# Performance work log

Hardware: AMD Instinct MI355X
Metric: run time of the kernel (lower is better)

Reference implementation:

```python
import math
import jax, jax.numpy as jnp
import numpy as np

N_HEAD = 12
LN_EPS = 1e-5

def _gelu(x):
    # NewGELU: tanh approximation
    c = math.sqrt(2.0 / math.pi)
    return 0.5 * x * (1.0 + jnp.tanh(c * (x + 0.044715 * x ** 3)))

def _ln(x, w, b):
    m = x.mean(-1, keepdims=True)
    v = x.var(-1, keepdims=True)
    return (x - m) / jnp.sqrt(v + LN_EPS) * w + b

def setup_inputs() -> dict:
    key = jax.random.key(0)
    ks = jax.random.split(key, 8)
    L, C, V, BS = 12, 768, 30522, 1024
    B, T = 4, 1024
    std = 0.02
    inp = {
        'idx': jax.random.randint(ks[0], (B, T), 0, V),
        'wte': jax.random.normal(ks[1], (V, C), jnp.float32) * std,
        'wpe': jax.random.normal(ks[2], (BS, C), jnp.float32) * std,
        'ln1_w': jnp.ones((L, C), jnp.float32),
        'ln1_b': jnp.zeros((L, C), jnp.float32),
        'attn_w': jax.random.normal(ks[3], (L, 3 * C, C), jnp.float32) * std,
        'attn_b': jnp.zeros((L, 3 * C), jnp.float32),
        'proj_w': jax.random.normal(ks[4], (L, C, C), jnp.float32) * (std / math.sqrt(2 * L)),
        'proj_b': jnp.zeros((L, C), jnp.float32),
        'ln2_w': jnp.ones((L, C), jnp.float32),
        'ln2_b': jnp.zeros((L, C), jnp.float32),
        'fc_w': jax.random.normal(ks[5], (L, 4 * C, C), jnp.float32) * std,
        'fc_b': jnp.zeros((L, 4 * C), jnp.float32),
        'mproj_w': jax.random.normal(ks[6], (L, C, 4 * C), jnp.float32) * (std / math.sqrt(2 * L)),
        'mproj_b': jnp.zeros((L, C), jnp.float32),
        'lnf_w': jnp.ones((C,), jnp.float32),
        'lnf_b': jnp.zeros((C,), jnp.float32),
        'lm_head_w': jax.random.normal(ks[7], (V, C), jnp.float32) * std,
    }
    return inp

def reference(idx, wte, wpe, ln1_w, ln1_b, attn_w, attn_b, proj_w, proj_b,
              ln2_w, ln2_b, fc_w, fc_b, mproj_w, mproj_b, lnf_w, lnf_b, lm_head_w):
    B, T = idx.shape
    C = wte.shape[1]
    H = N_HEAD
    D = C // H
    scale = 1.0 / math.sqrt(D)
    x = wte[idx] + wpe[:T][None]  # [B,T,C], drop is identity (p=0)

    def block(x, p):
        l1w, l1b, aw, ab, pw, pb, l2w, l2b, fw, fb, mw, mb = p
        h = _ln(x, l1w, l1b)
        qkv = jnp.einsum('btc,ec->bte', h, aw) + ab  # [B,T,3C]
        q, k, v = jnp.split(qkv, 3, axis=-1)
        q = q.reshape(B, T, H, D)
        k = k.reshape(B, T, H, D)
        v = v.reshape(B, T, H, D)
        att = jnp.einsum('bthd,bshd->bhts', q, k) * scale  # [B,H,T,T]
        att = jax.nn.softmax(att, axis=-1)  # mask=None: full attention
        y = jnp.einsum('bhts,bshd->bthd', att, v).reshape(B, T, C)
        x = x + jnp.einsum('btc,oc->bto', y, pw) + pb
        h = _gelu(jnp.einsum('btc,fc->btf', _ln(x, l2w, l2b), fw) + fb)
        x = x + jnp.einsum('btf,cf->btc', h, mw) + mb
        return x, None

    x, _ = jax.lax.scan(block, x, (ln1_w, ln1_b, attn_w, attn_b, proj_w, proj_b,
                                   ln2_w, ln2_b, fc_w, fc_b, mproj_w, mproj_b))
    x = _ln(x, lnf_w, lnf_b)
    logits = jnp.einsum('btc,vc->btv', x, lm_head_w)  # [B,T,V]
    return logits
```

## Files before the change

### kernel.cpp

```cpp
#include <hip/hip_runtime.h>
#include <hip/hip_bf16.h>
#include <math.h>

typedef __attribute__((ext_vector_type(8))) short short8;
typedef __attribute__((ext_vector_type(4))) float f32x4;

typedef unsigned short u16;

__device__ __forceinline__ u16 f2bf(float f) {
    union { float f; unsigned int u; } v; v.f = f;
    unsigned int u = v.u;
    unsigned int r = (u + 0x7fffu + ((u >> 16) & 1u)) >> 16;
    return (u16)r;
}
__device__ __forceinline__ float bf2f(u16 u) {
    union { unsigned int u; float f; } v; v.u = ((unsigned int)u) << 16;
    return v.f;
}

__device__ __forceinline__ void gload16(const void* g, void* l) {
    __builtin_amdgcn_global_load_lds(
        (const __attribute__((address_space(1))) void*)g,
        (__attribute__((address_space(3))) void*)l, 16, 0, 0);
}

__global__ __launch_bounds__(256) void castw_kernel(const float* __restrict__ src,
                                                    u16* __restrict__ dst,
                                                    long n, long npad) {
    long i = ((long)blockIdx.x * 256 + threadIdx.x) * 4;
    const long stride = (long)gridDim.x * 1024;
    for (; i < npad; i += stride) {
        ushort4 o;
        if (i < n) {
            float4 v = *reinterpret_cast<const float4*>(src + i);
            o.x = f2bf(v.x); o.y = f2bf(v.y); o.z = f2bf(v.z); o.w = f2bf(v.w);
        } else {
            o = make_ushort4(0, 0, 0, 0);
        }
        *reinterpret_cast<ushort4*>(dst + i) = o;
    }
}

__global__ __launch_bounds__(256) void embed_kernel(const int* __restrict__ idx,
                                                    const float* __restrict__ wte,
                                                    const float* __restrict__ wpe,
                                                    float* __restrict__ x) {
    const int row = blockIdx.x;
    const int tid = threadIdx.x;
    const int t = row & 1023;
    const int tok = idx[row];
    const float* we = wte + (size_t)tok * 768;
    const float* pe = wpe + (size_t)t * 768;
    float* xr = x + (size_t)row * 768;
    xr[tid]       = we[tid]       + pe[tid];
    xr[tid + 256] = we[tid + 256] + pe[tid + 256];
    xr[tid + 512] = we[tid + 512] + pe[tid + 512];
}

__global__ __launch_bounds__(256) void ln_kernel(const float* __restrict__ x,
                                                 const float* __restrict__ w,
                                                 const float* __restrict__ b,
                                                 u16* __restrict__ out) {
    const int row = blockIdx.x;
    const int tid = threadIdx.x;
    const float* xr = x + (size_t)row * 768;
    float v0 = xr[tid], v1 = xr[tid + 256], v2 = xr[tid + 512];
    float s = v0 + v1 + v2;
    float q = v0 * v0 + v1 * v1 + v2 * v2;
    #pragma unroll
    for (int off = 32; off >= 1; off >>= 1) {
        s += __shfl_xor(s, off);
        q += __shfl_xor(q, off);
    }
    __shared__ float rs[4], rq[4];
    const int wid = tid >> 6, lane = tid & 63;
    if (lane == 0) { rs[wid] = s; rq[wid] = q; }
    __syncthreads();
    s = rs[0] + rs[1] + rs[2] + rs[3];
    q = rq[0] + rq[1] + rq[2] + rq[3];
    const float mean = s * (1.f / 768.f);
    const float var = q * (1.f / 768.f) - mean * mean;
    const float rstd = rsqrtf(var + 1e-5f);
    u16* orow = out + (size_t)row * 768;
    orow[tid]       = f2bf((v0 - mean) * rstd * w[tid]       + b[tid]);
    orow[tid + 256] = f2bf((v1 - mean) * rstd * w[tid + 256] + b[tid + 256]);
    orow[tid + 512] = f2bf((v2 - mean) * rstd * w[tid + 512] + b[tid + 512]);
}

template<int EPI>
__global__ __launch_bounds__(256) void gemm_bb(
        const u16* __restrict__ A, int lda,
        const u16* __restrict__ B, int ldb,
        const float* __restrict__ bias,
        void* __restrict__ Cout, int ldc,
        int N, int K, int nmt,
        float* __restrict__ resid) {
    __shared__ __align__(16) u16 lds[2][2][128 * 32];
    const int tid = threadIdx.x;
    const int lane = tid & 63, wid = tid >> 6;
    const int nwg = gridDim.x;
    const int o = blockIdx.x;
    const int wg = (o & 7) * (nwg >> 3) + (o >> 3);
    const int m0 = (wg % nmt) * 128, n0 = (wg / nmt) * 128;

    const int wm = (wid >> 1) * 64, wn = (wid & 1) * 64;
    const int l16 = lane & 15, lk = (lane >> 4) * 8;

    const size_t a_off0 = (size_t)(m0 + (tid >> 2)) * lda + (tid & 3) * 8;
    const size_t a_off1 = a_off0 + (size_t)64 * lda;
    const size_t b_off0 = (size_t)(n0 + (tid >> 2)) * ldb + (tid & 3) * 8;
    const size_t b_off1 = b_off0 + (size_t)64 * ldb;
    const int ldst = tid * 8;

    f32x4 acc[4][4];
    #pragma unroll
    for (int i = 0; i < 4; i++)
        #pragma unroll
        for (int j = 0; j < 4; j++)
            acc[i][j] = (f32x4){0.f, 0.f, 0.f, 0.f};

    const int nk = K >> 5;
    gload16(A + a_off0, lds[0][0] + ldst);
    gload16(A + a_off1, lds[0][0] + ldst + 2048);
    gload16(B + b_off0, lds[0][1] + ldst);
    gload16(B + b_off1, lds[0][1] + ldst + 2048);

    for (int t = 0; t < nk; ++t) {
        if (t + 1 < nk) {
            u16* Ap = lds[(t + 1) & 1][0];
            u16* Bp = lds[(t + 1) & 1][1];
            const int k0 = (t + 1) << 5;
            gload16(A + a_off0 + k0, Ap + ldst);
            gload16(A + a_off1 + k0, Ap + ldst + 2048);
            gload16(B + b_off0 + k0, Bp + ldst);
            gload16(B + b_off1 + k0, Bp + ldst + 2048);
            asm volatile("s_waitcnt vmcnt(4)" ::: "memory");
        } else {
            asm volatile("s_waitcnt vmcnt(0)" ::: "memory");
        }
        __builtin_amdgcn_s_barrier();
        asm volatile("" ::: "memory");
        const u16* As = lds[t & 1][0];
        const u16* Bs = lds[t & 1][1];
        short8 af[4], bf[4];
        #pragma unroll
        for (int i = 0; i < 4; i++) {
            af[i] = *reinterpret_cast<const short8*>(&As[(wm + i * 16 + l16) * 32 + lk]);
            bf[i] = *reinterpret_cast<const short8*>(&Bs[(wn + i * 16 + l16) * 32 + lk]);
        }
        #pragma unroll
        for (int mi = 0; mi < 4; mi++)
            #pragma unroll
            for (int ni = 0; ni < 4; ni++)
                acc[mi][ni] = __builtin_amdgcn_mfma_f32_16x16x32_bf16(af[mi], bf[ni], acc[mi][ni], 0, 0, 0);
        asm volatile("" ::: "memory");
        __builtin_amdgcn_s_barrier();
    }

    if (EPI == 3) {
        float* ct = reinterpret_cast<float*>(&lds[0][0][0]) + wid * 1088;
        const int rw = (lane >> 4) * 4;
        const int rr = lane >> 2;
        const int rc = (lane & 3) * 16;
        #pragma unroll
        for (int mi = 0; mi < 4; mi++) {
            asm volatile("" ::: "memory");
            #pragma unroll
            for (int ni = 0; ni < 4; ni++)
                #pragma unroll
                for (int j = 0; j < 4; j++)
                    ct[(rw + j) * 68 + ni * 16 + l16] = acc[mi][ni][j];
            asm volatile("" ::: "memory");
            const int m = m0 + wm + mi * 16 + rr;
            const int nb = n0 + wn + rc;
            float* crow = (float*)Cout + (size_t)m * ldc + nb;
            #pragma unroll
            for (int q = 0; q < 4; q++) {
                const f32x4 v = *reinterpret_cast<const f32x4*>(&ct[rr * 68 + rc + q * 4]);
                if (nb + q * 4 + 3 < N) {
                    *reinterpret_cast<f32x4*>(crow + q * 4) = v;
                } else {
                    #pragma unroll
                    for (int e = 0; e < 4; e++)
                        if (nb + q * 4 + e < N) crow[q * 4 + e] = v[e];
                }
            }
        }
    } else {
        const int cb = n0 + wn + l16;
        const int rb = m0 + wm + (lane >> 4) * 4;
        #pragma unroll
        for (int ni = 0; ni < 4; ni++) {
            const int n = cb + ni * 16;
            const float bv = bias[n];
            #pragma unroll
            for (int mi = 0; mi < 4; mi++) {
                #pragma unroll
                for (int j = 0; j < 4; j++) {
                    const int m = rb + mi * 16 + j;
                    float v = acc[mi][ni][j] + bv;
                    if (EPI == 0) {
                        ((u16*)Cout)[(size_t)m * ldc + n] = f2bf(v);
                    } else if (EPI == 1) {
                        resid[(size_t)m * ldc + n] += v;
                    } else {
                        const float t = tanhf(0.7978845608028654f * (v + 0.044715f * v * v * v));
                        ((u16*)Cout)[(size_t)m * ldc + n] = f2bf(0.5f * v * (1.f + t));
                    }
                }
            }
        }
    }
}

template<int EPI>
__global__ __launch_bounds__(256, 2) void gemm_bt(
        const u16* __restrict__ A, int lda,
        const float* __restrict__ B, int ldb,
        const float* __restrict__ bias,
        void* __restrict__ Cout, int ldc,
        int M, int N, int K,
        float* __restrict__ resid) {
    __shared__ __align__(16) u16 As[128][40];
    __shared__ __align__(16) u16 Bs[128][40];
    const int tid = threadIdx.x;
    const int lane = tid & 63, wid = tid >> 6;
    const int m0 = blockIdx.y * 128, n0 = blockIdx.x * 128;
    const int wm = (wid >> 1) * 64, wn = (wid & 1) * 64;
    const int l16 = lane & 15, lk = (lane >> 4) * 8;

    f32x4 acc[4][4];
    #pragma unroll
    for (int i = 0; i < 4; i++)
        #pragma unroll
        for (int j = 0; j < 4; j++)
            acc[i][j] = (f32x4){0.f, 0.f, 0.f, 0.f};

    for (int k0 = 0; k0 < K; k0 += 32) {
        #pragma unroll
        for (int p = 0; p < 2; p++) {
            const int e = p * 256 + tid;
            const int r = e >> 2, c = e & 3;
            uint4 v = *reinterpret_cast<const uint4*>(A + (size_t)(m0 + r) * lda + k0 + c * 8);
            *reinterpret_cast<uint4*>(&As[r][c * 8]) = v;
        }
        #pragma unroll
        for (int p = 0; p < 4; p++) {
            const int e = p * 256 + tid;
            const int r = e >> 3, c = e & 7;
            float4 v = make_float4(0.f, 0.f, 0.f, 0.f);
            if (n0 + r < N)
                v = *reinterpret_cast<const float4*>(B + (size_t)(n0 + r) * ldb + k0 + c * 4);
            ushort4 hv;
            hv.x = f2bf(v.x); hv.y = f2bf(v.y); hv.z = f2bf(v.z); hv.w = f2bf(v.w);
            *reinterpret_cast<ushort4*>(&Bs[r][c * 4]) = hv;
        }
        __syncthreads();
        short8 af[4], bfr[4];
        #pragma unroll
        for (int i = 0; i < 4; i++) {
            af[i]  = *reinterpret_cast<const short8*>(&As[wm + i * 16 + l16][lk]);
            bfr[i] = *reinterpret_cast<const short8*>(&Bs[wn + i * 16 + l16][lk]);
        }
        #pragma unroll
        for (int mi = 0; mi < 4; mi++)
            #pragma unroll
            for (int ni = 0; ni < 4; ni++)
                acc[mi][ni] = __builtin_amdgcn_mfma_f32_16x16x32_bf16(af[mi], bfr[ni], acc[mi][ni], 0, 0, 0);
        __syncthreads();
    }

    const int cb = n0 + wn + l16;
    const int rb = m0 + wm + (lane >> 4) * 4;
    #pragma unroll
    for (int ni = 0; ni < 4; ni++) {
        const int n = cb + ni * 16;
        if (n >= N) continue;
        float bv = 0.f;
        if (EPI != 3) bv = bias[n];
        #pragma unroll
        for (int mi = 0; mi < 4; mi++) {
            #pragma unroll
            for (int j = 0; j < 4; j++) {
                const int m = rb + mi * 16 + j;
                float v = acc[mi][ni][j] + bv;
                if (EPI == 0) {
                    ((u16*)Cout)[(size_t)m * ldc + n] = f2bf(v);
                } else if (EPI == 1) {
                    resid[(size_t)m * ldc + n] += v;
                } else if (EPI == 2) {
                    const float t = tanhf(0.7978845608028654f * (v + 0.044715f * v * v * v));
                    ((u16*)Cout)[(size_t)m * ldc + n] = f2bf(0.5f * v * (1.f + t));
                } else {
                    ((float*)Cout)[(size_t)m * ldc + n] = v;
                }
            }
        }
    }
}

__global__ __launch_bounds__(256, 2) void attn_mfma_kernel(const u16* __restrict__ qkv,
                                                           u16* __restrict__ y) {
    __shared__ __align__(16) u16 Qs[64][72];
    __shared__ __align__(16) u16 Ks[64][72];
    __shared__ __align__(16) u16 Vt[64][72];
    __shared__ __align__(16) u16 Ps[4][16][72];

    const int tid = threadIdx.x;
    const int lane = tid & 63, wid = tid >> 6;
    const int l16 = lane & 15, lk = (lane >> 4) * 8;
    const int qt = blockIdx.x, h = blockIdx.y, b = blockIdx.z;

    const size_t base = (size_t)b * 1024 * 2304;
    const u16* qp = qkv + base + (size_t)(qt * 64) * 2304 + h * 64;
    const u16* kp = qkv + base + 768  + h * 64;
    const u16* vp = qkv + base + 1536 + h * 64;

    #pragma unroll
    for (int p = 0; p < 2; p++) {
        const int e = p * 256 + tid;
        const int rr = e >> 3, c8 = e & 7;
        *reinterpret_cast<uint4*>(&Qs[rr][c8 * 8]) =
            *reinterpret_cast<const uint4*>(qp + (size_t)rr * 2304 + c8 * 8);
    }
    __syncthreads();

    short8 qf[2];
    #pragma unroll
    for (int kk = 0; kk < 2; kk++)
        qf[kk] = *reinterpret_cast<const short8*>(&Qs[wid * 16 + l16][kk * 32 + lk]);

    f32x4 o_acc[4];
    #pragma unroll
    for (int i = 0; i < 4; i++) o_acc[i] = (f32x4){0.f, 0.f, 0.f, 0.f};
    float l_part[4] = {0.f, 0.f, 0.f, 0.f};

    for (int s0 = 0; s0 < 1024; s0 += 64) {
        __syncthreads();
        #pragma unroll
        for (int p = 0; p < 2; p++) {
            const int e = p * 256 + tid;
            const int rr = e >> 3, c8 = e & 7;
            *reinterpret_cast<uint4*>(&Ks[rr][c8 * 8]) =
                *reinterpret_cast<const uint4*>(kp + (size_t)(s0 + rr) * 2304 + c8 * 8);
        }
        #pragma unroll
        for (int p = 0; p < 2; p++) {
            const int e = p * 256 + tid;
            const int s2 = e >> 4;
            const int dq = e & 15;
            const int s = s2 * 2;
            ushort4 v0 = *reinterpret_cast<const ushort4*>(vp + (size_t)(s0 + s) * 2304 + dq * 4);
            ushort4 v1 = *reinterpret_cast<const ushort4*>(vp + (size_t)(s0 + s + 1) * 2304 + dq * 4);
            *reinterpret_cast<ushort2*>(&Vt[dq * 4 + 0][s]) = make_ushort2(v0.x, v1.x);
            *reinterpret_cast<ushort2*>(&Vt[dq * 4 + 1][s]) = make_ushort2(v0.y, v1.y);
            *reinterpret_cast<ushort2*>(&Vt[dq * 4 + 2][s]) = make_ushort2(v0.z, v1.z);
            *reinterpret_cast<ushort2*>(&Vt[dq * 4 + 3][s]) = make_ushort2(v0.w, v1.w);
        }
        __syncthreads();

        f32x4 sa[4];
        #pragma unroll
        for (int i = 0; i < 4; i++) sa[i] = (f32x4){0.f, 0.f, 0.f, 0.f};
        #pragma unroll
        for (int nj = 0; nj < 4; nj++) {
            #pragma unroll
            for (int kk = 0; kk < 2; kk++) {
                short8 kf = *reinterpret_cast<const short8*>(&Ks[nj * 16 + l16][kk * 32 + lk]);
                sa[nj] = __builtin_amdgcn_mfma_f32_16x16x32_bf16(qf[kk], kf, sa[nj], 0, 0, 0);
            }
        }

        #pragma unroll
        for (int nj = 0; nj < 4; nj++) {
            #pragma unroll
            for (int r = 0; r < 4; r++) {
                const float pv = __expf(sa[nj][r] * 0.125f);
                l_part[r] += pv;
                Ps[wid][(lane >> 4) * 4 + r][nj * 16 + l16] = f2bf(pv);
            }
        }

        short8 pa[2];
        #pragma unroll
        for (int kk = 0; kk < 2; kk++)
            pa[kk] = *reinterpret_cast<const short8*>(&Ps[wid][l16][kk * 32 + lk]);
        #pragma unroll
        for (int nd = 0; nd < 4; nd++) {
            #pragma unroll
            for (int kk = 0; kk < 2; kk++) {
                short8 vf = *reinterpret_cast<const short8*>(&Vt[nd * 16 + l16][kk * 32 + lk]);
                o_acc[nd] = __builtin_amdgcn_mfma_f32_16x16x32_bf16(pa[kk], vf, o_acc[nd], 0, 0, 0);
            }
        }
    }

    float inv[4];
    #pragma unroll
    for (int r = 0; r < 4; r++) {
        float s = l_part[r];
        #pragma unroll
        for (int off = 8; off >= 1; off >>= 1) s += __shfl_xor(s, off);
        inv[r] = 1.f / s;
    }
    const int rowb = b * 1024 + qt * 64 + wid * 16 + (lane >> 4) * 4;
    #pragma unroll
    for (int nd = 0; nd < 4; nd++) {
        const int col = h * 64 + nd * 16 + l16;
        #pragma unroll
        for (int r = 0; r < 4; r++) {
            y[(size_t)(rowb + r) * 768 + col] = f2bf(o_acc[nd][r] * inv[r]);
        }
    }
}

extern "C" void kernel_launch(void* const* d_in, const int* in_sizes, int n_in,
                              void* d_out, int out_size, void* d_ws, size_t ws_size,
                              hipStream_t stream) {
    (void)in_sizes; (void)n_in; (void)out_size;
    const int*   idx    = (const int*)d_in[0];
    const float* wte    = (const float*)d_in[1];
    const float* wpe    = (const float*)d_in[2];
    const float* ln1w   = (const float*)d_in[3];
    const float* ln1b   = (const float*)d_in[4];
    const float* attnw  = (const float*)d_in[5];
    const float* attnb  = (const float*)d_in[6];
    const float* projw  = (const float*)d_in[7];
    const float* projb  = (const float*)d_in[8];
    const float* ln2w   = (const float*)d_in[9];
    const float* ln2b   = (const float*)d_in[10];
    const float* fcw    = (const float*)d_in[11];
    const float* fcb    = (const float*)d_in[12];
    const float* mprojw = (const float*)d_in[13];
    const float* mprojb = (const float*)d_in[14];
    const float* lnfw   = (const float*)d_in[15];
    const float* lnfb   = (const float*)d_in[16];
    const float* lmw    = (const float*)d_in[17];
    float* out = (float*)d_out;

    char* p = (char*)d_ws;
    size_t used = 0;
    auto take = [&](size_t bytes) { char* q = p + used; used += (bytes + 255) & ~(size_t)255; return q; };
    float* x      = (float*)take((size_t)4096 * 768 * 4);
    u16*   a_bf   = (u16*)take((size_t)4096 * 768 * 2);
    u16*   qkv_bf = (u16*)take((size_t)4096 * 2304 * 2);
    u16*   hid_bf = (u16*)take((size_t)4096 * 3072 * 2);
    u16*   w_lm   = (u16*)take((size_t)30592 * 768 * 2);
    const bool castLm = used <= ws_size;
    u16*   w_attn = (u16*)take((size_t)12 * 2304 * 768 * 2);
    u16*   w_proj = (u16*)take((size_t)12 * 768 * 768 * 2);
    u16*   w_fc   = (u16*)take((size_t)12 * 3072 * 768 * 2);
    u16*   w_mprj = (u16*)take((size_t)12 * 768 * 3072 * 2);
    const bool castAll = used <= ws_size;

    embed_kernel<<<4096, 256, 0, stream>>>(idx, wte, wpe, x);

    if (castLm)
        castw_kernel<<<2048, 256, 0, stream>>>(lmw, w_lm, (long)30522 * 768, (long)30592 * 768);
    if (castAll) {
        castw_kernel<<<2048, 256, 0, stream>>>(attnw,  w_attn, (long)12 * 2304 * 768, (long)12 * 2304 * 768);
        castw_kernel<<<2048, 256, 0, stream>>>(projw,  w_proj, (long)12 * 768 * 768,  (long)12 * 768 * 768);
        castw_kernel<<<2048, 256, 0, stream>>>(fcw,    w_fc,   (long)12 * 3072 * 768, (long)12 * 3072 * 768);
        castw_kernel<<<2048, 256, 0, stream>>>(mprojw, w_mprj, (long)12 * 768 * 3072, (long)12 * 768 * 3072);
    }

    for (int l = 0; l < 12; l++) {
        ln_kernel<<<4096, 256, 0, stream>>>(x, ln1w + l * 768, ln1b + l * 768, a_bf);
        if (castAll) {
            gemm_bb<0><<<32 * 18, 256, 0, stream>>>(
                a_bf, 768, w_attn + (size_t)l * 2304 * 768, 768, attnb + l * 2304,
                (void*)qkv_bf, 2304, 2304, 768, 32, nullptr);
        } else {
            gemm_bt<0><<<dim3(18, 32), 256, 0, stream>>>(
                a_bf, 768, attnw + (size_t)l * 2304 * 768, 768, attnb + l * 2304,
                (void*)qkv_bf, 2304, 4096, 2304, 768, nullptr);
        }
        attn_mfma_kernel<<<dim3(16, 12, 4), 256, 0, stream>>>(qkv_bf, a_bf);
        if (castAll) {
            gemm_bb<1><<<32 * 6, 256, 0, stream>>>(
                a_bf, 768, w_proj + (size_t)l * 768 * 768, 768, projb + l * 768,
                nullptr, 768, 768, 768, 32, x);
        } else {
            gemm_bt<1><<<dim3(6, 32), 256, 0, stream>>>(
                a_bf, 768, projw + (size_t)l * 768 * 768, 768, projb + l * 768,
                nullptr, 768, 4096, 768, 768, x);
        }
        ln_kernel<<<4096, 256, 0, stream>>>(x, ln2w + l * 768, ln2b + l * 768, a_bf);
        if (castAll) {
            gemm_bb<2><<<32 * 24, 256, 0, stream>>>(
                a_bf, 768, w_fc + (size_t)l * 3072 * 768, 768, fcb + l * 3072,
                (void*)hid_bf, 3072, 3072, 768, 32, nullptr);
            gemm_bb<1><<<32 * 6, 256, 0, stream>>>(
                hid_bf, 3072, w_mprj + (size_t)l * 768 * 3072, 3072, mprojb + l * 768,
                nullptr, 768, 768, 3072, 32, x);
        } else {
            gemm_bt<2><<<dim3(24, 32), 256, 0, stream>>>(
                a_bf, 768, fcw + (size_t)l * 3072 * 768, 768, fcb + l * 3072,
                (void*)hid_bf, 3072, 4096, 3072, 768, nullptr);
            gemm_bt<1><<<dim3(6, 32), 256, 0, stream>>>(
                hid_bf, 3072, mprojw + (size_t)l * 768 * 3072, 3072, mprojb + l * 768,
                nullptr, 768, 4096, 768, 3072, x);
        }
    }

    ln_kernel<<<4096, 256, 0, stream>>>(x, lnfw, lnfb, a_bf);
    if (castLm) {
        gemm_bb<3><<<32 * 239, 256, 0, stream>>>(
            a_bf, 768, w_lm, 768, nullptr, (void*)out, 30522, 30522, 768, 32, nullptr);
    } else {
        gemm_bt<3><<<dim3(239, 32), 256, 0, stream>>>(
            a_bf, 768, lmw, 768, nullptr, (void*)out, 30522, 4096, 30522, 768, nullptr);
    }
}
```

Before: 3.115 ms.

## Add 256x128 eight-wave GEMM with XOR-swizzled LDS for QKV, FC and LM head

Adds a gemm_big kernel that runs 512 threads over a 256x128 output tile, so each B tile loaded into LDS is shared by twice as many rows. It is used for the QKV, FC and LM-head GEMMs. Both GEMM kernels now XOR-swizzle the 16-byte chunk position in LDS to reduce bank conflicts on the MFMA fragment reads. gemm_bb loses its EPI 3 path. The LM-head epilogue in gemm_big adds a barrier per mi iteration because the staging area overlaps LDS used by other waves.

```diff
diff --git a/kernel.cpp b/kernel.cpp
--- a/kernel.cpp
+++ b/kernel.cpp
@@ -85,6 +85,130 @@
     orow[tid]       = f2bf((v0 - mean) * rstd * w[tid]       + b[tid]);
     orow[tid + 256] = f2bf((v1 - mean) * rstd * w[tid + 256] + b[tid + 256]);
     orow[tid + 512] = f2bf((v2 - mean) * rstd * w[tid + 512] + b[tid + 512]);
+}
+
+template<int EPI>
+__global__ __launch_bounds__(512) void gemm_big(
+        const u16* __restrict__ A, int lda,
+        const u16* __restrict__ B, int ldb,
+        const float* __restrict__ bias,
+        void* __restrict__ Cout, int ldc,
+        int N, int K, int nmt) {
+    __shared__ __align__(16) u16 lds[2][384 * 32];
+    const int tid = threadIdx.x;
+    const int lane = tid & 63, wid = tid >> 6;
+    const int nwg = gridDim.x;
+    const int o = blockIdx.x;
+    const int wg = (o & 7) * (nwg >> 3) + (o >> 3);
+    const int m0 = (wg % nmt) * 256, n0 = (wg / nmt) * 128;
+
+    const int wm = (wid >> 1) * 64, wn = (wid & 1) * 64;
+    const int l16 = lane & 15;
+    const int qid = lane >> 4;
+    const int xq8 = ((qid ^ (l16 & 3)) * 8);
+
+    const int ar = tid >> 2, aq = (tid & 3) ^ (ar & 3);
+    const size_t a_src0 = (size_t)(m0 + ar) * lda + aq * 8;
+    const size_t a_src1 = (size_t)(m0 + ar + 128) * lda + aq * 8;
+    const int br = tid >> 2, bq = (tid & 3) ^ (br & 3);
+    const size_t b_src = (size_t)(n0 + br) * ldb + bq * 8;
+
+    f32x4 acc[4][4];
+    #pragma unroll
+    for (int i = 0; i < 4; i++)
+        #pragma unroll
+        for (int j = 0; j < 4; j++)
+            acc[i][j] = (f32x4){0.f, 0.f, 0.f, 0.f};
+
+    const int nk = K >> 5;
+    gload16(A + a_src0, lds[0] + tid * 8);
+    gload16(A + a_src1, lds[0] + tid * 8 + 4096);
+    gload16(B + b_src,  lds[0] + tid * 8 + 8192);
+
+    for (int t = 0; t < nk; ++t) {
+        if (t + 1 < nk) {
+            u16* buf = lds[(t + 1) & 1];
+            const int k0 = (t + 1) << 5;
+            gload16(A + a_src0 + k0, buf + tid * 8);
+            gload16(A + a_src1 + k0, buf + tid * 8 + 4096);
+            gload16(B + b_src + k0,  buf + tid * 8 + 8192);
+            asm volatile("s_waitcnt vmcnt(3)" ::: "memory");
+        } else {
+            asm volatile("s_waitcnt vmcnt(0)" ::: "memory");
+        }
+        __builtin_amdgcn_s_barrier();
+        asm volatile("" ::: "memory");
+        const u16* As = lds[t & 1];
+        const u16* Bs = lds[t & 1] + 8192;
+        short8 af[4], bf[4];
+        #pragma unroll
+        for (int i = 0; i < 4; i++) {
+            af[i] = *reinterpret_cast<const short8*>(&As[(wm + i * 16 + l16) * 32 + xq8]);
+            bf[i] = *reinterpret_cast<const short8*>(&Bs[(wn + i * 16 + l16) * 32 + xq8]);
+        }
+        #pragma unroll
+        for (int mi = 0; mi < 4; mi++)
+            #pragma unroll
+            for (int ni = 0; ni < 4; ni++)
+                acc[mi][ni] = __builtin_amdgcn_mfma_f32_16x16x32_bf16(af[mi], bf[ni], acc[mi][ni], 0, 0, 0);
+        asm volatile("" ::: "memory");
+        __builtin_amdgcn_s_barrier();
+    }
+
+    if (EPI == 3) {
+        float* ct = reinterpret_cast<float*>(&lds[0][0]) + wid * 1088;
+        const int rw = (lane >> 4) * 4;
+        const int rr = lane >> 2;
+        const int rc = (lane & 3) * 16;
+        #pragma unroll
+        for (int mi = 0; mi < 4; mi++) {
+            asm volatile("" ::: "memory");
+            #pragma unroll
+            for (int ni = 0; ni < 4; ni++)
+                #pragma unroll
+                for (int j = 0; j < 4; j++)
+                    ct[(rw + j) * 68 + ni * 16 + l16] = acc[mi][ni][j];
+            asm volatile("" ::: "memory");
+            const int m = m0 + wm + mi * 16 + rr;
+            const int nb = n0 + wn + rc;
+            float* crow = (float*)Cout + (size_t)m * ldc + nb;
+            #pragma unroll
+            for (int q = 0; q < 4; q++) {
+                const f32x4 v = *reinterpret_cast<const f32x4*>(&ct[rr * 68 + rc + q * 4]);
+                if (nb + q * 4 + 3 < N) {
+                    *reinterpret_cast<f32x4*>(crow + q * 4) = v;
+                } else {
+                    #pragma unroll
+                    for (int e = 0; e < 4; e++)
+                        if (nb + q * 4 + e < N) crow[q * 4 + e] = v[e];
+                }
+            }
+            asm volatile("" ::: "memory");
+            __builtin_amdgcn_s_barrier();
+        }
+    } else {
+        const int cb = n0 + wn + l16;
+        const int rb = m0 + wm + (lane >> 4) * 4;
+        #pragma unroll
+        for (int ni = 0; ni < 4; ni++) {
+            const int n = cb + ni * 16;
+            const float bv = bias[n];
+            #pragma unroll
+            for (int mi = 0; mi < 4; mi++) {
+                #pragma unroll
+                for (int j = 0; j < 4; j++) {
+                    const int m = rb + mi * 16 + j;
+                    float v = acc[mi][ni][j] + bv;
+                    if (EPI == 0) {
+                        ((u16*)Cout)[(size_t)m * ldc + n] = f2bf(v);
+                    } else {
+                        const float t = tanhf(0.7978845608028654f * (v + 0.044715f * v * v * v));
+                        ((u16*)Cout)[(size_t)m * ldc + n] = f2bf(0.5f * v * (1.f + t));
+                    }
+                }
+            }
+        }
+    }
 }
 
 template<int EPI>
@@ -104,13 +228,15 @@
     const int m0 = (wg % nmt) * 128, n0 = (wg / nmt) * 128;
 
     const int wm = (wid >> 1) * 64, wn = (wid & 1) * 64;
-    const int l16 = lane & 15, lk = (lane >> 4) * 8;
-
-    const size_t a_off0 = (size_t)(m0 + (tid >> 2)) * lda + (tid & 3) * 8;
-    const size_t a_off1 = a_off0 + (size_t)64 * lda;
-    const size_t b_off0 = (size_t)(n0 + (tid >> 2)) * ldb + (tid & 3) * 8;
-    const size_t b_off1 = b_off0 + (size_t)64 * ldb;
-    const int ldst = tid * 8;
+    const int l16 = lane & 15;
+    const int qid = lane >> 4;
+    const int xq8 = ((qid ^ (l16 & 3)) * 8);
+
+    const int r0 = tid >> 2, q0 = (tid & 3) ^ (r0 & 3);
+    const size_t a_src0 = (size_t)(m0 + r0) * lda + q0 * 8;
+    const size_t a_src1 = (size_t)(m0 + r0 + 64) * lda + q0 * 8;
+    const size_t b_src0 = (size_t)(n0 + r0) * ldb + q0 * 8;
+    const size_t b_src1 = (size_t)(n0 + r0 + 64) * ldb + q0 * 8;
 
     f32x4 acc[4][4];
     #pragma unroll
@@ -120,20 +246,20 @@
             acc[i][j] = (f32x4){0.f, 0.f, 0.f, 0.f};
 
     const int nk = K >> 5;
-    gload16(A + a_off0, lds[0][0] + ldst);
-    gload16(A + a_off1, lds[0][0] + ldst + 2048);
-    gload16(B + b_off0, lds[0][1] + ldst);
-    gload16(B + b_off1, lds[0][1] + ldst + 2048);
+    gload16(A + a_src0, lds[0][0] + tid * 8);
+    gload16(A + a_src1, lds[0][0] + tid * 8 + 2048);
+    gload16(B + b_src0, lds[0][1] + tid * 8);
+    gload16(B + b_src1, lds[0][1] + tid * 8 + 2048);
 
     for (int t = 0; t < nk; ++t) {
         if (t + 1 < nk) {
             u16* Ap = lds[(t + 1) & 1][0];
             u16* Bp = lds[(t + 1) & 1][1];
             const int k0 = (t + 1) << 5;
-            gload16(A + a_off0 + k0, Ap + ldst);
-            gload16(A + a_off1 + k0, Ap + ldst + 2048);
-            gload16(B + b_off0 + k0, Bp + ldst);
-            gload16(B + b_off1 + k0, Bp + ldst + 2048);
+            gload16(A + a_src0 + k0, Ap + tid * 8);
+            gload16(A + a_src1 + k0, Ap + tid * 8 + 2048);
+            gload16(B + b_src0 + k0, Bp + tid * 8);
+            gload16(B + b_src1 + k0, Bp + tid * 8 + 2048);
             asm volatile("s_waitcnt vmcnt(4)" ::: "memory");
         } else {
             asm volatile("s_waitcnt vmcnt(0)" ::: "memory");
@@ -145,8 +271,8 @@
         short8 af[4], bf[4];
         #pragma unroll
         for (int i = 0; i < 4; i++) {
-            af[i] = *reinterpret_cast<const short8*>(&As[(wm + i * 16 + l16) * 32 + lk]);
-            bf[i] = *reinterpret_cast<const short8*>(&Bs[(wn + i * 16 + l16) * 32 + lk]);
+            af[i] = *reinterpret_cast<const short8*>(&As[(wm + i * 16 + l16) * 32 + xq8]);
+            bf[i] = *reinterpret_cast<const short8*>(&Bs[(wn + i * 16 + l16) * 32 + xq8]);
         }
         #pragma unroll
         for (int mi = 0; mi < 4; mi++)
@@ -157,56 +283,25 @@
         __builtin_amdgcn_s_barrier();
     }
 
-    if (EPI == 3) {
-        float* ct = reinterpret_cast<float*>(&lds[0][0][0]) + wid * 1088;
-        const int rw = (lane >> 4) * 4;
-        const int rr = lane >> 2;
-        const int rc = (lane & 3) * 16;
+    const int cb = n0 + wn + l16;
+    const int rb = m0 + wm + (lane >> 4) * 4;
+    #pragma unroll
+    for (int ni = 0; ni < 4; ni++) {
+        const int n = cb + ni * 16;
+        const float bv = bias[n];
         #pragma unroll
         for (int mi = 0; mi < 4; mi++) {
-            asm volatile("" ::: "memory");
-            #pragma unroll
-            for (int ni = 0; ni < 4; ni++)
-                #pragma unroll
-                for (int j = 0; j < 4; j++)
-                    ct[(rw + j) * 68 + ni * 16 + l16] = acc[mi][ni][j];
-            asm volatile("" ::: "memory");
-            const int m = m0 + wm + mi * 16 + rr;
-            const int nb = n0 + wn + rc;
-            float* crow = (float*)Cout + (size_t)m * ldc + nb;
-            #pragma unroll
-            for (int q = 0; q < 4; q++) {
-                const f32x4 v = *reinterpret_cast<const f32x4*>(&ct[rr * 68 + rc + q * 4]);
-                if (nb + q * 4 + 3 < N) {
-                    *reinterpret_cast<f32x4*>(crow + q * 4) = v;
+            #pragma unroll
+            for (int j = 0; j < 4; j++) {
+                const int m = rb + mi * 16 + j;
+                float v = acc[mi][ni][j] + bv;
+                if (EPI == 1) {
+                    resid[(size_t)m * ldc + n] += v;
+                } else if (EPI == 0) {
+                    ((u16*)Cout)[(size_t)m * ldc + n] = f2bf(v);
                 } else {
-                    #pragma unroll
-                    for (int e = 0; e < 4; e++)
-                        if (nb + q * 4 + e < N) crow[q * 4 + e] = v[e];
-                }
-            }
-        }
-    } else {
-        const int cb = n0 + wn + l16;
-        const int rb = m0 + wm + (lane >> 4) * 4;
-        #pragma unroll
-        for (int ni = 0; ni < 4; ni++) {
-            const int n = cb + ni * 16;
-            const float bv = bias[n];
-            #pragma unroll
-            for (int mi = 0; mi < 4; mi++) {
-                #pragma unroll
-                for (int j = 0; j < 4; j++) {
-                    const int m = rb + mi * 16 + j;
-                    float v = acc[mi][ni][j] + bv;
-                    if (EPI == 0) {
-                        ((u16*)Cout)[(size_t)m * ldc + n] = f2bf(v);
-                    } else if (EPI == 1) {
-                        resid[(size_t)m * ldc + n] += v;
-                    } else {
-                        const float t = tanhf(0.7978845608028654f * (v + 0.044715f * v * v * v));
-                        ((u16*)Cout)[(size_t)m * ldc + n] = f2bf(0.5f * v * (1.f + t));
-                    }
+                    const float t = tanhf(0.7978845608028654f * (v + 0.044715f * v * v * v));
+                    ((u16*)Cout)[(size_t)m * ldc + n] = f2bf(0.5f * v * (1.f + t));
                 }
             }
         }
@@ -467,9 +562,9 @@
     for (int l = 0; l < 12; l++) {
         ln_kernel<<<4096, 256, 0, stream>>>(x, ln1w + l * 768, ln1b + l * 768, a_bf);
         if (castAll) {
-            gemm_bb<0><<<32 * 18, 256, 0, stream>>>(
+            gemm_big<0><<<16 * 18, 512, 0, stream>>>(
                 a_bf, 768, w_attn + (size_t)l * 2304 * 768, 768, attnb + l * 2304,
-                (void*)qkv_bf, 2304, 2304, 768, 32, nullptr);
+                (void*)qkv_bf, 2304, 2304, 768, 16);
         } else {
             gemm_bt<0><<<dim3(18, 32), 256, 0, stream>>>(
                 a_bf, 768, attnw + (size_t)l * 2304 * 768, 768, attnb + l * 2304,
@@ -487,9 +582,9 @@
         }
         ln_kernel<<<4096, 256, 0, stream>>>(x, ln2w + l * 768, ln2b + l * 768, a_bf);
         if (castAll) {
-            gemm_bb<2><<<32 * 24, 256, 0, stream>>>(
+            gemm_big<2><<<16 * 24, 512, 0, stream>>>(
                 a_bf, 768, w_fc + (size_t)l * 3072 * 768, 768, fcb + l * 3072,
-                (void*)hid_bf, 3072, 3072, 768, 32, nullptr);
+                (void*)hid_bf, 3072, 3072, 768, 16);
             gemm_bb<1><<<32 * 6, 256, 0, stream>>>(
                 hid_bf, 3072, w_mprj + (size_t)l * 768 * 3072, 3072, mprojb + l * 768,
                 nullptr, 768, 768, 3072, 32, x);
@@ -505,8 +600,8 @@
 
     ln_kernel<<<4096, 256, 0, stream>>>(x, lnfw, lnfb, a_bf);
     if (castLm) {
-        gemm_bb<3><<<32 * 239, 256, 0, stream>>>(
-            a_bf, 768, w_lm, 768, nullptr, (void*)out, 30522, 30522, 768, 32, nullptr);
+        gemm_big<3><<<16 * 239, 512, 0, stream>>>(
+            a_bf, 768, w_lm, 768, nullptr, (void*)out, 30522, 30522, 768, 16);
     } else {
         gemm_bt<3><<<dim3(239, 32), 256, 0, stream>>>(
             a_bf, 768, lmw, 768, nullptr, (void*)out, 30522, 4096, 30522, 768, nullptr);
```

Measured after the change: 3.031 ms. 2.7% less time.
